# Kernel optimization log

Measured on AMD Instinct MI355X. Metric: run time of the kernel, lower is better.

Reference implementation:

```python
import jax, jax.numpy as jnp
import numpy as np

DIM = 1024
N_HEADS = 16
HEAD_DIM = DIM // N_HEADS


def setup_inputs() -> dict:
    key = jax.random.key(0)
    ks = jax.random.split(key, 9)
    s = 0.02
    return {
        "x": jax.random.normal(ks[0], (2, 2048, DIM), dtype=jnp.float32),
        "Wq": jax.random.normal(ks[1], (DIM, DIM), dtype=jnp.float32) * s,
        "bq": jax.random.normal(ks[2], (DIM,), dtype=jnp.float32) * s,
        "Wk": jax.random.normal(ks[3], (DIM, DIM), dtype=jnp.float32) * s,
        "bk": jax.random.normal(ks[4], (DIM,), dtype=jnp.float32) * s,
        "Wv": jax.random.normal(ks[5], (DIM, DIM), dtype=jnp.float32) * s,
        "bv": jax.random.normal(ks[6], (DIM,), dtype=jnp.float32) * s,
        "Wo": jax.random.normal(ks[7], (DIM, DIM), dtype=jnp.float32) * s,
        "bo": jax.random.normal(ks[8], (DIM,), dtype=jnp.float32) * s,
    }


def reference(x, Wq, bq, Wk, bk, Wv, bv, Wo, bo):
    B, T, C = x.shape
    # QKV projections, split heads -> [B, H, T, D]
    def split_heads(t):
        return t.reshape(B, T, N_HEADS, HEAD_DIM).transpose(0, 2, 1, 3)
    q = split_heads(x @ Wq + bq)
    k = split_heads(x @ Wk + bk)
    v = split_heads(x @ Wv + bv)
    scale = 1.0 / jnp.sqrt(jnp.float32(HEAD_DIM))
    scores = jnp.einsum("bhqd,bhkd->bhqk", q, k) * scale  # [B,H,T,T]
    causal = jnp.tril(jnp.ones((T, T), dtype=bool))  # True = keep
    scores = jnp.where(causal, scores, jnp.float32(-jnp.inf))
    weights = jax.nn.softmax(scores, axis=-1)
    ctx = jnp.einsum("bhqk,bhkd->bhqd", weights, v)
    ctx = ctx.transpose(0, 2, 1, 3).reshape(B, T, C)
    return ctx @ Wo + bo
```

## Files before the change

### kernel.cpp

```cpp
#include <hip/hip_runtime.h>
#include <hip/hip_bf16.h>
#include <stdint.h>

#define DIM    1024
#define SEQ    2048
#define NB     2
#define NH     16
#define HD     64
#define NROWS  (NB*SEQ)

typedef unsigned short u16;
typedef __attribute__((ext_vector_type(8))) short bf16x8;
typedef __attribute__((ext_vector_type(4))) float f32x4;
typedef __attribute__((ext_vector_type(4))) unsigned short u16x4;

#define NEG_INF (-__builtin_inff())

__device__ __forceinline__ u16 f2bf(float f) {
    union { float f; uint32_t u; } x; x.f = f;
    uint32_t r = x.u + 0x7FFFu + ((x.u >> 16) & 1u);
    return (u16)(r >> 16);
}

__device__ __forceinline__ uint32_t cvtpk(float a, float b) {
    uint32_t r;
    asm volatile("v_cvt_pk_bf16_f32 %0, %1, %2" : "=v"(r) : "v"(a), "v"(b));
    return r;
}

__device__ __forceinline__ void gload_lds16(const void* g, void* l) {
    __builtin_amdgcn_global_load_lds(
        (const __attribute__((address_space(1))) void*)g,
        (__attribute__((address_space(3))) void*)l, 16, 0, 0);
}

__global__ __launch_bounds__(256)
void cvt_x(const float* __restrict__ in, u16* __restrict__ out)
{
    size_t i = (size_t)blockIdx.x * 256 + threadIdx.x;
    float4 f = *(const float4*)&in[i * 4];
    u16x4 o = { f2bf(f.x), f2bf(f.y), f2bf(f.z), f2bf(f.w) };
    *(u16x4*)&out[i * 4] = o;
}

__global__ __launch_bounds__(256)
void cvt_w(const float* __restrict__ Wq, const float* __restrict__ Wk,
           const float* __restrict__ Wv, const float* __restrict__ Wo,
           u16* __restrict__ Wqt, u16* __restrict__ Wkt,
           u16* __restrict__ Wvt, u16* __restrict__ Wot)
{
    __shared__ u16 Ws[64][68];
    const int z = blockIdx.z;
    const float* W = z == 0 ? Wq : z == 1 ? Wk : z == 2 ? Wv : Wo;
    u16* Wt        = z == 0 ? Wqt : z == 1 ? Wkt : z == 2 ? Wvt : Wot;
    const int k0 = blockIdx.x * 64;
    const int n0 = blockIdx.y * 64;
    const int tid = threadIdx.x;

    #pragma unroll
    for (int it = 0; it < 4; ++it) {
        int idx = tid + it * 256;
        int r = idx >> 4, cq = idx & 15;
        float4 f = *(const float4*)&W[(size_t)(k0 + r) * DIM + n0 + cq * 4];
        u16x4 o = { f2bf(f.x), f2bf(f.y), f2bf(f.z), f2bf(f.w) };
        *(u16x4*)&Ws[r][cq * 4] = o;
    }
    __syncthreads();
    #pragma unroll
    for (int it = 0; it < 4; ++it) {
        int idx = tid + it * 256;
        int rr = idx >> 4, cq = idx & 15;
        u16x4 o = { Ws[cq*4+0][rr], Ws[cq*4+1][rr], Ws[cq*4+2][rr], Ws[cq*4+3][rr] };
        *(u16x4*)&Wt[(size_t)(n0 + rr) * DIM + k0 + cq * 4] = o;
    }
}

template<int MODE>
__global__ __launch_bounds__(256)
void gemm_mfma(const u16* __restrict__ A,
               const u16* __restrict__ Wt0, const u16* __restrict__ Wt1,
               const u16* __restrict__ Wt2,
               const float* __restrict__ b0, const float* __restrict__ b1,
               const float* __restrict__ b2,
               void* __restrict__ o0, void* __restrict__ o1, void* __restrict__ o2)
{
    __shared__ __align__(16) uint8_t lds[32768];
    uint8_t* Asb = lds;
    uint8_t* Bsb = lds + 16384;

    const int tid  = threadIdx.x;
    const int wid  = tid >> 6, lane = tid & 63;
    const int lr   = lane & 15, lg = lane >> 4;
    const int wr   = wid >> 1, wc = wid & 1;

    const int r0 = blockIdx.x * 128;
    const int c0 = blockIdx.y * 128;

    const u16* Wt; const float* bias; u16* obf = nullptr; float* ofp = nullptr;
    int cw; float qscale = 1.0f;
    if (MODE == 0) {
        int sel = c0 >> 10;
        cw  = c0 & 1023;
        Wt   = sel == 0 ? Wt0 : sel == 1 ? Wt1 : Wt2;
        bias = sel == 0 ? b0  : sel == 1 ? b1  : b2;
        obf  = (u16*)(sel == 0 ? o0 : sel == 1 ? o1 : o2);
        if (sel == 0) qscale = 0.125f * 1.44269504088896f;
    } else {
        cw = c0; Wt = Wt0; bias = b0; ofp = (float*)o0;
    }

    f32x4 acc[4][4] = {};

    for (int k0 = 0; k0 < DIM; k0 += 64) {
        __syncthreads();
        #pragma unroll
        for (int seg = 0; seg < 4; ++seg) {
            int o   = seg * 4096 + tid * 16;
            int row = o >> 7;
            int sch = ((o >> 4) & 7) ^ (row & 7);
            gload_lds16((const uint8_t*)A  + ((size_t)(r0 + row) << 11) + (k0 << 1) + (sch << 4),
                        Asb + seg * 4096 + (wid << 10) + (lane << 4));
            gload_lds16((const uint8_t*)Wt + ((size_t)(cw + row) << 11) + (k0 << 1) + (sch << 4),
                        Bsb + seg * 4096 + (wid << 10) + (lane << 4));
        }
        __syncthreads();

        __builtin_amdgcn_s_setprio(1);
        #pragma unroll
        for (int kk = 0; kk < 2; ++kk) {
            bf16x8 a[4], b[4];
            #pragma unroll
            for (int i = 0; i < 4; ++i) {
                int ar = wr * 64 + i * 16 + lr;
                a[i] = *(const bf16x8*)(Asb + ar * 128 + ((((kk << 2) | lg) ^ (ar & 7)) << 4));
                int br = wc * 64 + i * 16 + lr;
                b[i] = *(const bf16x8*)(Bsb + br * 128 + ((((kk << 2) | lg) ^ (br & 7)) << 4));
            }
            #pragma unroll
            for (int i = 0; i < 4; ++i)
                #pragma unroll
                for (int j = 0; j < 4; ++j)
                    acc[i][j] = __builtin_amdgcn_mfma_f32_16x16x32_bf16(a[i], b[j], acc[i][j], 0, 0, 0);
        }
        __builtin_amdgcn_s_setprio(0);
    }

    #pragma unroll
    for (int j = 0; j < 4; ++j) {
        int colw = wc * 64 + j * 16 + lr;
        float bv = bias[cw + colw];
        #pragma unroll
        for (int i = 0; i < 4; ++i) {
            #pragma unroll
            for (int r = 0; r < 4; ++r) {
                float val = (acc[i][j][r] + bv) * qscale;
                int row = r0 + wr * 64 + i * 16 + lg * 4 + r;
                if (MODE == 0) {
                    int col = cw + colw;
                    int h = col >> 6, d = col & 63;
                    int bb = row >> 11, t = row & (SEQ - 1);
                    obf[((((size_t)bb * NH + h) * SEQ + t) << 6) + d] = f2bf(val);
                } else {
                    ofp[((size_t)row << 10) + c0 + colw] = val;
                }
            }
        }
    }
}

__global__ __launch_bounds__(256)
void attn_mfma(const u16* __restrict__ q, const u16* __restrict__ k,
               const u16* __restrict__ v, u16* __restrict__ ctx)
{
    __shared__ __align__(16) uint8_t lds[24576];
    uint8_t* Qs = lds;
    uint8_t* Ks = lds + 8192;
    uint8_t* Vt = lds + 16384;

    const int tid = threadIdx.x;
    const int wid = tid >> 6, lane = tid & 63;
    const int lr  = lane & 15, lg = lane >> 4;

    const int n  = blockIdx.x;
    const int j4 = n >> 8;
    const int c  = n & 255;
    const int ch = c >> 5;
    const int bh = c & 31;
    const int qt = (j4 == 0) ? ch : (j4 == 1) ? (15 - ch)
                 : (j4 == 2) ? (16 + ch) : (31 - ch);

    const size_t hb = (size_t)bh * SEQ * HD;
    const int q0 = qt * 64;

    #pragma unroll
    for (int seg = 0; seg < 2; ++seg) {
        int o = seg * 4096 + tid * 16;
        int row = o >> 7;
        int sch = ((o >> 4) & 7) ^ (row & 7);
        gload_lds16((const uint8_t*)(q + hb) + (size_t)(q0 + row) * 128 + (sch << 4),
                    Qs + seg * 4096 + (wid << 10) + (lane << 4));
    }

    const int vp = tid >> 3;
    const int vg = tid & 7;
    const int vj  = vp >> 3;
    const int vlg = (vp >> 1) & 3;
    const int vrr = (vp & 1) * 2;
    const int vslot = (vj & 1) * 32 + vlg * 8 + ((vj >> 1) << 2) + vrr;

    const u16* vbase = v + hb + ((size_t)(2 * vp) << 6) + vg * 8;

    bf16x8 vpre0 = *(const bf16x8*)(vbase);
    bf16x8 vpre1 = *(const bf16x8*)(vbase + 64);

    f32x4 acc[4] = {};
    float m_own = NEG_INF;
    float l_own = 0.f;
    bf16x8 aQ0, aQ1;

    for (int kt = 0; kt <= qt; ++kt) {
        __syncthreads();
        #pragma unroll
        for (int seg = 0; seg < 2; ++seg) {
            int o = seg * 4096 + tid * 16;
            int row = o >> 7;
            int sch = ((o >> 4) & 7) ^ (row & 7);
            gload_lds16((const uint8_t*)(k + hb) + (size_t)(kt * 64 + row) * 128 + (sch << 4),
                        Ks + seg * 4096 + (wid << 10) + (lane << 4));
        }
        {
            #pragma unroll
            for (int i = 0; i < 8; ++i) {
                int d = vg * 8 + i;
                int swzd = (d ^ (d >> 3)) & 7;
                uint32_t w = (uint32_t)(u16)vpre0[i] | ((uint32_t)(u16)vpre1[i] << 16);
                *(uint32_t*)(Vt + d * 128 + ((((vslot >> 3) ^ swzd) << 4))
                             + ((vslot & 7) << 1)) = w;
            }
        }
        __syncthreads();

        if (kt < qt) {
            const u16* vsrc = vbase + ((size_t)(kt + 1) << 12);
            vpre0 = *(const bf16x8*)(vsrc);
            vpre1 = *(const bf16x8*)(vsrc + 64);
        }

        if (kt == 0) {
            int qr = wid * 16 + lr;
            aQ0 = *(const bf16x8*)(Qs + qr * 128 + ((lg       ^ (qr & 7)) << 4));
            aQ1 = *(const bf16x8*)(Qs + qr * 128 + (((4 | lg) ^ (qr & 7)) << 4));
        }

        f32x4 s[4];
        __builtin_amdgcn_s_setprio(1);
        #pragma unroll
        for (int j = 0; j < 4; ++j) {
            int krow = j * 16 + lr;
            bf16x8 b0 = *(const bf16x8*)(Ks + krow * 128 + ((lg       ^ (krow & 7)) << 4));
            bf16x8 b1 = *(const bf16x8*)(Ks + krow * 128 + (((4 | lg) ^ (krow & 7)) << 4));
            f32x4 z = {0.f, 0.f, 0.f, 0.f};
            z    = __builtin_amdgcn_mfma_f32_16x16x32_bf16(b0, aQ0, z, 0, 0, 0);
            s[j] = __builtin_amdgcn_mfma_f32_16x16x32_bf16(b1, aQ1, z, 0, 0, 0);
        }
        __builtin_amdgcn_s_setprio(0);

        if (kt == qt) {
            #pragma unroll
            for (int j = 0; j < 4; ++j)
                #pragma unroll
                for (int r = 0; r < 4; ++r)
                    if (j * 16 + lg * 4 + r > wid * 16 + lr) s[j][r] = NEG_INF;
        }

        float rm = NEG_INF;
        #pragma unroll
        for (int j = 0; j < 4; ++j) {
            float a = fmaxf(fmaxf(s[j][0], s[j][1]), fmaxf(s[j][2], s[j][3]));
            rm = fmaxf(rm, a);
        }
        rm = fmaxf(rm, __shfl_xor(rm, 16));
        rm = fmaxf(rm, __shfl_xor(rm, 32));

        if (!__all(rm <= m_own + 8.f)) {
            float mnew = fmaxf(m_own, rm);
            float aown = exp2f(m_own - mnew);
            m_own = mnew;
            l_own *= aown;
            float ar[4];
            #pragma unroll
            for (int r = 0; r < 4; ++r) ar[r] = __shfl(aown, lg * 4 + r);
            #pragma unroll
            for (int ni = 0; ni < 4; ++ni)
                #pragma unroll
                for (int r = 0; r < 4; ++r)
                    acc[ni][r] *= ar[r];
        }

        float rs = 0.f;
        #pragma unroll
        for (int j = 0; j < 4; ++j)
            #pragma unroll
            for (int r = 0; r < 4; ++r) {
                float p = exp2f(s[j][r] - m_own);
                s[j][r] = p;
                rs += p;
            }
        rs += __shfl_xor(rs, 16);
        rs += __shfl_xor(rs, 32);
        l_own += rs;

        union { uint32_t u[4]; bf16x8 h; } P0, P1;
        P0.u[0] = cvtpk(s[0][0], s[0][1]); P0.u[1] = cvtpk(s[0][2], s[0][3]);
        P0.u[2] = cvtpk(s[2][0], s[2][1]); P0.u[3] = cvtpk(s[2][2], s[2][3]);
        P1.u[0] = cvtpk(s[1][0], s[1][1]); P1.u[1] = cvtpk(s[1][2], s[1][3]);
        P1.u[2] = cvtpk(s[3][0], s[3][1]); P1.u[3] = cvtpk(s[3][2], s[3][3]);

        __builtin_amdgcn_s_setprio(1);
        #pragma unroll
        for (int ni = 0; ni < 4; ++ni) {
            int vrow = ni * 16 + lr;
            int swzd = (vrow ^ (vrow >> 3)) & 7;
            bf16x8 vb0 = *(const bf16x8*)(Vt + vrow * 128 + ((lg       ^ swzd) << 4));
            bf16x8 vb1 = *(const bf16x8*)(Vt + vrow * 128 + (((4 | lg) ^ swzd) << 4));
            acc[ni] = __builtin_amdgcn_mfma_f32_16x16x32_bf16(P0.h, vb0, acc[ni], 0, 0, 0);
            acc[ni] = __builtin_amdgcn_mfma_f32_16x16x32_bf16(P1.h, vb1, acc[ni], 0, 0, 0);
        }
        __builtin_amdgcn_s_setprio(0);
    }

    float rinv = 1.f / l_own;
    float rl[4];
    #pragma unroll
    for (int r = 0; r < 4; ++r) rl[r] = __shfl(rinv, lg * 4 + r);

    const int b = bh >> 4, h = bh & 15;
    #pragma unroll
    for (int r = 0; r < 4; ++r) {
        int t = q0 + wid * 16 + lg * 4 + r;
        size_t base = (((size_t)b * SEQ + t) << 10) + (h << 6);
        #pragma unroll
        for (int ni = 0; ni < 4; ++ni)
            ctx[base + ni * 16 + lr] = f2bf(acc[ni][r] * rl[r]);
    }
}

extern "C" void kernel_launch(void* const* d_in, const int* in_sizes, int n_in,
                              void* d_out, int out_size, void* d_ws, size_t ws_size,
                              hipStream_t stream)
{
    (void)in_sizes; (void)n_in; (void)out_size; (void)ws_size;
    const float* x  = (const float*)d_in[0];
    const float* Wq = (const float*)d_in[1];
    const float* bq = (const float*)d_in[2];
    const float* Wk = (const float*)d_in[3];
    const float* bk = (const float*)d_in[4];
    const float* Wv = (const float*)d_in[5];
    const float* bv = (const float*)d_in[6];
    const float* Wo = (const float*)d_in[7];
    const float* bo = (const float*)d_in[8];

    u16* ws = (u16*)d_ws;
    const size_t M1 = (size_t)1024 * 1024;
    const size_t M4 = (size_t)NROWS * DIM;
    u16* xb  = ws;
    u16* wqt = ws + M4;
    u16* wkt = wqt + M1;
    u16* wvt = wkt + M1;
    u16* wot = wvt + M1;
    u16* qb  = wot + M1;
    u16* kb  = qb + M4;
    u16* vb  = kb + M4;
    u16* cb  = vb + M4;

    cvt_x<<<dim3(4096), dim3(256), 0, stream>>>(x, xb);
    cvt_w<<<dim3(16, 16, 4), dim3(256), 0, stream>>>(Wq, Wk, Wv, Wo, wqt, wkt, wvt, wot);
    gemm_mfma<0><<<dim3(32, 24), dim3(256), 0, stream>>>(
        xb, wqt, wkt, wvt, bq, bk, bv, qb, kb, vb);
    attn_mfma<<<dim3(1024), dim3(256), 0, stream>>>(qb, kb, vb, cb);
    gemm_mfma<1><<<dim3(32, 8), dim3(256), 0, stream>>>(
        cb, wot, nullptr, nullptr, bo, nullptr, nullptr, d_out, nullptr, nullptr);
}
```

Measured before the change: 195.1 us.

## Split causal attention KV range into two chunks with a combine kernel

Each query tile's causal key range is split into two halves processed by separate blocks, which write partial fp32 outputs plus running max and sum to workspace. A new combine kernel merges the two partials and writes the bf16 context. This doubles the block count to balance the triangular workload and lift occupancy, at the cost of an extra launch and extra global traffic for the partials. Q fragments now load straight into registers instead of through LDS, and K is register-prefetched instead of using async LDS loads, which shrinks shared memory. The split path only runs when the workspace is large enough, otherwise the old path is used.

Measured after the change: 191.3 us. Within noise of the previous version (-1.9%).

```diff
diff --git a/kernel.cpp b/kernel.cpp
--- a/kernel.cpp
+++ b/kernel.cpp
@@ -168,38 +168,49 @@
     }
 }
 
+template<int SPLIT>
 __global__ __launch_bounds__(256)
 void attn_mfma(const u16* __restrict__ q, const u16* __restrict__ k,
-               const u16* __restrict__ v, u16* __restrict__ ctx)
-{
-    __shared__ __align__(16) uint8_t lds[24576];
-    uint8_t* Qs = lds;
-    uint8_t* Ks = lds + 8192;
-    uint8_t* Vt = lds + 16384;
+               const u16* __restrict__ v, u16* __restrict__ ctx,
+               float* __restrict__ pO, float* __restrict__ pML)
+{
+    __shared__ __align__(16) uint8_t lds[16384];
+    uint8_t* Ks = lds;
+    uint8_t* Vt = lds + 8192;
 
     const int tid = threadIdx.x;
     const int wid = tid >> 6, lane = tid & 63;
     const int lr  = lane & 15, lg = lane >> 4;
 
-    const int n  = blockIdx.x;
-    const int j4 = n >> 8;
-    const int c  = n & 255;
-    const int ch = c >> 5;
-    const int bh = c & 31;
-    const int qt = (j4 == 0) ? ch : (j4 == 1) ? (15 - ch)
-                 : (j4 == 2) ? (16 + ch) : (31 - ch);
+    const int n = blockIdx.x;
+    int bh, qt, k_lo, k_hi, pidx = 0;
+    if (SPLIT) {
+        bh = n & 31;
+        int u = n >> 5;
+        qt = u >> 1;
+        int chunk = u & 1;
+        int T = qt + 1, hh = (T + 1) >> 1;
+        k_lo = chunk ? hh : 0;
+        k_hi = chunk ? T : hh;
+        pidx = (((bh << 5) | qt) << 1) | chunk;
+    } else {
+        int j4 = n >> 8, c = n & 255, ch = c >> 5;
+        bh = c & 31;
+        qt = (j4 == 0) ? ch : (j4 == 1) ? (15 - ch)
+           : (j4 == 2) ? (16 + ch) : (31 - ch);
+        k_lo = 0; k_hi = qt + 1;
+    }
 
     const size_t hb = (size_t)bh * SEQ * HD;
     const int q0 = qt * 64;
 
-    #pragma unroll
-    for (int seg = 0; seg < 2; ++seg) {
-        int o = seg * 4096 + tid * 16;
-        int row = o >> 7;
-        int sch = ((o >> 4) & 7) ^ (row & 7);
-        gload_lds16((const uint8_t*)(q + hb) + (size_t)(q0 + row) * 128 + (sch << 4),
-                    Qs + seg * 4096 + (wid << 10) + (lane << 4));
-    }
+    const u16* qrow = q + hb + ((size_t)(q0 + wid * 16 + lr) << 6);
+    bf16x8 aQ0 = *(const bf16x8*)(qrow + lg * 8);
+    bf16x8 aQ1 = *(const bf16x8*)(qrow + 32 + lg * 8);
+
+    const int kr  = tid >> 2;
+    const int kc0 = (tid & 3) * 2;
+    const u16* kbase = k + hb + ((size_t)kr << 6) + kc0 * 8;
 
     const int vp = tid >> 3;
     const int vg = tid & 7;
@@ -207,49 +218,43 @@
     const int vlg = (vp >> 1) & 3;
     const int vrr = (vp & 1) * 2;
     const int vslot = (vj & 1) * 32 + vlg * 8 + ((vj >> 1) << 2) + vrr;
-
     const u16* vbase = v + hb + ((size_t)(2 * vp) << 6) + vg * 8;
 
-    bf16x8 vpre0 = *(const bf16x8*)(vbase);
-    bf16x8 vpre1 = *(const bf16x8*)(vbase + 64);
+    bf16x8 kpre0 = {}, kpre1 = {}, vpre0 = {}, vpre1 = {};
+    if (k_lo < k_hi) {
+        const u16* ks = kbase + ((size_t)k_lo << 12);
+        kpre0 = *(const bf16x8*)(ks);
+        kpre1 = *(const bf16x8*)(ks + 8);
+        const u16* vs = vbase + ((size_t)k_lo << 12);
+        vpre0 = *(const bf16x8*)(vs);
+        vpre1 = *(const bf16x8*)(vs + 64);
+    }
 
     f32x4 acc[4] = {};
     float m_own = NEG_INF;
     float l_own = 0.f;
-    bf16x8 aQ0, aQ1;
-
-    for (int kt = 0; kt <= qt; ++kt) {
+
+    for (int kt = k_lo; kt < k_hi; ++kt) {
         __syncthreads();
-        #pragma unroll
-        for (int seg = 0; seg < 2; ++seg) {
-            int o = seg * 4096 + tid * 16;
-            int row = o >> 7;
-            int sch = ((o >> 4) & 7) ^ (row & 7);
-            gload_lds16((const uint8_t*)(k + hb) + (size_t)(kt * 64 + row) * 128 + (sch << 4),
-                        Ks + seg * 4096 + (wid << 10) + (lane << 4));
-        }
-        {
-            #pragma unroll
-            for (int i = 0; i < 8; ++i) {
-                int d = vg * 8 + i;
-                int swzd = (d ^ (d >> 3)) & 7;
-                uint32_t w = (uint32_t)(u16)vpre0[i] | ((uint32_t)(u16)vpre1[i] << 16);
-                *(uint32_t*)(Vt + d * 128 + ((((vslot >> 3) ^ swzd) << 4))
-                             + ((vslot & 7) << 1)) = w;
-            }
+        *(bf16x8*)(Ks + kr * 128 + ((kc0       ^ (kr & 7)) << 4)) = kpre0;
+        *(bf16x8*)(Ks + kr * 128 + (((kc0 + 1) ^ (kr & 7)) << 4)) = kpre1;
+        #pragma unroll
+        for (int i = 0; i < 8; ++i) {
+            int d = vg * 8 + i;
+            int swzd = (d ^ (d >> 3)) & 7;
+            uint32_t w = (uint32_t)(u16)vpre0[i] | ((uint32_t)(u16)vpre1[i] << 16);
+            *(uint32_t*)(Vt + d * 128 + ((((vslot >> 3) ^ swzd) << 4))
+                         + ((vslot & 7) << 1)) = w;
         }
         __syncthreads();
 
-        if (kt < qt) {
-            const u16* vsrc = vbase + ((size_t)(kt + 1) << 12);
-            vpre0 = *(const bf16x8*)(vsrc);
-            vpre1 = *(const bf16x8*)(vsrc + 64);
-        }
-
-        if (kt == 0) {
-            int qr = wid * 16 + lr;
-            aQ0 = *(const bf16x8*)(Qs + qr * 128 + ((lg       ^ (qr & 7)) << 4));
-            aQ1 = *(const bf16x8*)(Qs + qr * 128 + (((4 | lg) ^ (qr & 7)) << 4));
+        if (kt + 1 < k_hi) {
+            const u16* ks = kbase + ((size_t)(kt + 1) << 12);
+            kpre0 = *(const bf16x8*)(ks);
+            kpre1 = *(const bf16x8*)(ks + 8);
+            const u16* vs = vbase + ((size_t)(kt + 1) << 12);
+            vpre0 = *(const bf16x8*)(vs);
+            vpre1 = *(const bf16x8*)(vs + 64);
         }
 
         f32x4 s[4];
@@ -329,27 +334,81 @@
         __builtin_amdgcn_s_setprio(0);
     }
 
-    float rinv = 1.f / l_own;
-    float rl[4];
+    if (SPLIT) {
+        float* Op = pO + (size_t)pidx * 4096;
+        #pragma unroll
+        for (int r = 0; r < 4; ++r) {
+            int row = wid * 16 + lg * 4 + r;
+            #pragma unroll
+            for (int ni = 0; ni < 4; ++ni)
+                Op[row * 64 + ni * 16 + lr] = acc[ni][r];
+        }
+        if (lg == 0) {
+            pML[pidx * 128 + wid * 16 + lr]      = m_own;
+            pML[pidx * 128 + 64 + wid * 16 + lr] = l_own;
+        }
+    } else {
+        float rinv = 1.f / l_own;
+        float rl[4];
+        #pragma unroll
+        for (int r = 0; r < 4; ++r) rl[r] = __shfl(rinv, lg * 4 + r);
+        const int b = bh >> 4, h = bh & 15;
+        #pragma unroll
+        for (int r = 0; r < 4; ++r) {
+            int t = q0 + wid * 16 + lg * 4 + r;
+            size_t base = (((size_t)b * SEQ + t) << 10) + (h << 6);
+            #pragma unroll
+            for (int ni = 0; ni < 4; ++ni)
+                ctx[base + ni * 16 + lr] = f2bf(acc[ni][r] * rl[r]);
+        }
+    }
+}
+
+__global__ __launch_bounds__(256)
+void attn_combine(const float* __restrict__ pO, const float* __restrict__ pML,
+                  u16* __restrict__ ctx)
+{
+    int gid  = blockIdx.x * 256 + threadIdx.x;
+    int rg   = gid >> 2;
+    int dseg = gid & 3;
+    int bh = rg >> 11;
+    int qt = (rg >> 6) & 31;
+    int r  = rg & 63;
+    int p0 = ((bh << 5) | qt) << 1;
+
+    float m0 = pML[p0 * 128 + r],       l0 = pML[p0 * 128 + 64 + r];
+    float m1 = pML[(p0 + 1) * 128 + r], l1 = pML[(p0 + 1) * 128 + 64 + r];
+    float m  = fmaxf(m0, m1);
+    float s0 = exp2f(m0 - m), s1 = exp2f(m1 - m);
+    float rl = 1.f / (l0 * s0 + l1 * s1);
+
+    const float* O0 = pO + (size_t)p0 * 4096 + r * 64 + dseg * 16;
+    const float* O1 = O0 + 4096;
+
+    int b = bh >> 4, h = bh & 15, t = qt * 64 + r;
+    u16* dst = ctx + (((size_t)b * SEQ + t) << 10) + (h << 6) + dseg * 16;
+
+    u16x4 o[4];
     #pragma unroll
-    for (int r = 0; r < 4; ++r) rl[r] = __shfl(rinv, lg * 4 + r);
-
-    const int b = bh >> 4, h = bh & 15;
-    #pragma unroll
-    for (int r = 0; r < 4; ++r) {
-        int t = q0 + wid * 16 + lg * 4 + r;
-        size_t base = (((size_t)b * SEQ + t) << 10) + (h << 6);
-        #pragma unroll
-        for (int ni = 0; ni < 4; ++ni)
-            ctx[base + ni * 16 + lr] = f2bf(acc[ni][r] * rl[r]);
-    }
+    for (int i = 0; i < 4; ++i) {
+        float4 a = *(const float4*)&O0[i * 4];
+        float4 c = *(const float4*)&O1[i * 4];
+        o[i].x = f2bf((a.x * s0 + c.x * s1) * rl);
+        o[i].y = f2bf((a.y * s0 + c.y * s1) * rl);
+        o[i].z = f2bf((a.z * s0 + c.z * s1) * rl);
+        o[i].w = f2bf((a.w * s0 + c.w * s1) * rl);
+    }
+    *(u16x4*)(dst)      = o[0];
+    *(u16x4*)(dst + 4)  = o[1];
+    *(u16x4*)(dst + 8)  = o[2];
+    *(u16x4*)(dst + 12) = o[3];
 }
 
 extern "C" void kernel_launch(void* const* d_in, const int* in_sizes, int n_in,
                               void* d_out, int out_size, void* d_ws, size_t ws_size,
                               hipStream_t stream)
 {
-    (void)in_sizes; (void)n_in; (void)out_size; (void)ws_size;
+    (void)in_sizes; (void)n_in; (void)out_size;
     const float* x  = (const float*)d_in[0];
     const float* Wq = (const float*)d_in[1];
     const float* bq = (const float*)d_in[2];
@@ -372,12 +431,23 @@
     u16* kb  = qb + M4;
     u16* vb  = kb + M4;
     u16* cb  = vb + M4;
+    float* pO  = (float*)(cb + M4);
+    float* pML = pO + (size_t)2048 * 4096;
+
+    const size_t need = (size_t)(cb + M4 - ws) * 2
+                      + (size_t)2048 * 4096 * 4 + (size_t)2048 * 128 * 4;
+    const bool split = ws_size >= need;
 
     cvt_x<<<dim3(4096), dim3(256), 0, stream>>>(x, xb);
     cvt_w<<<dim3(16, 16, 4), dim3(256), 0, stream>>>(Wq, Wk, Wv, Wo, wqt, wkt, wvt, wot);
     gemm_mfma<0><<<dim3(32, 24), dim3(256), 0, stream>>>(
         xb, wqt, wkt, wvt, bq, bk, bv, qb, kb, vb);
-    attn_mfma<<<dim3(1024), dim3(256), 0, stream>>>(qb, kb, vb, cb);
+    if (split) {
+        attn_mfma<1><<<dim3(2048), dim3(256), 0, stream>>>(qb, kb, vb, nullptr, pO, pML);
+        attn_combine<<<dim3(1024), dim3(256), 0, stream>>>(pO, pML, cb);
+    } else {
+        attn_mfma<0><<<dim3(1024), dim3(256), 0, stream>>>(qb, kb, vb, cb, nullptr, nullptr);
+    }
     gemm_mfma<1><<<dim3(32, 8), dim3(256), 0, stream>>>(
         cb, wot, nullptr, nullptr, bo, nullptr, nullptr, d_out, nullptr, nullptr);
 }
```
